# Optimization experiments

Measured on AMD Instinct MI355X. Metric: run time of the kernel, lower is better.

The kernel has to match this reference:

```python
import jax, jax.numpy as jnp
import numpy as np

B, N, E, H = 8, 2000, 20, 128


def setup_inputs() -> dict:
    key = jax.random.key(0)
    ks = jax.random.split(key, 9)
    s = 1.0 / np.sqrt(H)
    return {
        "x": jax.random.normal(ks[0], (B, N, H), dtype=jnp.float32),
        "e": jax.random.normal(ks[1], (B, N * E, H), dtype=jnp.float32),
        "Wu": jax.random.uniform(ks[2], (H, H), jnp.float32, -s, s),
        "bu": jax.random.uniform(ks[3], (H,), jnp.float32, -s, s),
        "Wv": jax.random.uniform(ks[4], (H, H), jnp.float32, -s, s),
        "bv": jax.random.uniform(ks[5], (H,), jnp.float32, -s, s),
        "We": jax.random.uniform(ks[6], (H, H), jnp.float32, -s, s),
        "be": jax.random.uniform(ks[7], (H,), jnp.float32, -s, s),
        "edge_index": jax.random.randint(ks[8], (B, N * E), 0, N, dtype=jnp.int32),
        "n_edges": E,
    }


def reference(x, e, Wu, bu, Wv, bv, We, be, edge_index, n_edges):
    b, n, h = x.shape
    Ux = x @ Wu + bu                      # [B, N, H] node self-embedding
    Vx = x @ Wv + bv                      # [B, N, H] neighbor embedding
    Ve = e @ We + be                      # [B, N*E, H] edge embedding
    # softmax over the n_edges axis per (node, channel)
    Ve = jax.nn.softmax(Ve.reshape(b, n, n_edges, h), axis=2)
    # gather neighbor features along node axis via edge_index
    Vx_g = jnp.take_along_axis(Vx, edge_index[..., None], axis=1)  # [B, N*E, H]
    to = (Ve * Vx_g.reshape(b, n, n_edges, h)).sum(axis=2)          # [B, N, H]
    return Ux + to
```

## Files before the change

kernel.cpp:

```cpp
#include <hip/hip_runtime.h>

#define B_   8
#define NN   2000
#define EE   20
#define HH   128
#define BN   (B_*NN)
#define NE   (NN*EE)

typedef unsigned short ushort_t;
typedef __bf16 bf16x8 __attribute__((ext_vector_type(8)));
typedef float  f32x4  __attribute__((ext_vector_type(4)));
typedef float  f4     __attribute__((ext_vector_type(4)));
typedef unsigned short us8 __attribute__((ext_vector_type(8)));
typedef unsigned short us4 __attribute__((ext_vector_type(4)));

union FragU { us8 u; bf16x8 b; };

__device__ __forceinline__ float b2f(ushort_t v) {
    union { unsigned int i; float f; } c; c.i = ((unsigned int)v) << 16; return c.f;
}
__device__ __forceinline__ ushort_t f2b(float f) {
    union { float f; unsigned int i; } c; c.f = f;
    unsigned int r = (c.i + 0x7FFFu + ((c.i >> 16) & 1u)) >> 16;
    return (ushort_t)r;
}

__global__ __launch_bounds__(256, 2) void k1_embed(
    const float* __restrict__ x,
    const float* __restrict__ Wu, const float* __restrict__ bu,
    const float* __restrict__ Wv, const float* __restrict__ bv,
    ushort_t* __restrict__ Uxb, ushort_t* __restrict__ Vxb)
{
    __shared__ __align__(16) ushort_t As[128 * 136];

    const int tid  = threadIdx.x;
    const int lane = tid & 63;
    const int wave = tid >> 6;
    const int wm = wave >> 1, wn = wave & 1;
    const int q  = lane >> 4, ln = lane & 15;
    const int m0 = blockIdx.x * 128;
    const int sel = blockIdx.y;
    const float* W    = sel ? Wv : Wu;
    const float* bias = sel ? bv : bu;
    ushort_t* dst = sel ? Vxb : Uxb;

    for (int c = tid; c < 128 * 32; c += 256) {
        int row = c >> 5, col = (c & 31) * 4;
        f4 v = *(const f4*)(x + (size_t)(m0 + row) * HH + col);
        us4 pk;
#pragma unroll
        for (int r = 0; r < 4; ++r) pk[r] = f2b(v[r]);
        *(us4*)(&As[row * 136 + col]) = pk;
    }

    FragU bf[4][4];
#pragma unroll
    for (int ki = 0; ki < 4; ++ki)
#pragma unroll
        for (int tn = 0; tn < 4; ++tn) {
            int n = wn * 64 + tn * 16 + ln;
            us8 tmp;
#pragma unroll
            for (int i = 0; i < 8; ++i) tmp[i] = f2b(W[(ki * 32 + q * 8 + i) * HH + n]);
            bf[ki][tn].u = tmp;
        }

    f32x4 acc[4][4];
#pragma unroll
    for (int tm = 0; tm < 4; ++tm)
#pragma unroll
        for (int tn = 0; tn < 4; ++tn) acc[tm][tn] = (f32x4){0.f, 0.f, 0.f, 0.f};

    __syncthreads();

#pragma unroll
    for (int ki = 0; ki < 4; ++ki) {
        FragU af[4];
#pragma unroll
        for (int tm = 0; tm < 4; ++tm) {
            int row = wm * 64 + tm * 16 + ln;
            af[tm].u = *(const us8*)(&As[row * 136 + ki * 32 + q * 8]);
        }
#pragma unroll
        for (int tm = 0; tm < 4; ++tm)
#pragma unroll
            for (int tn = 0; tn < 4; ++tn)
                acc[tm][tn] = __builtin_amdgcn_mfma_f32_16x16x32_bf16(
                    af[tm].b, bf[ki][tn].b, acc[tm][tn], 0, 0, 0);
    }

#pragma unroll
    for (int tn = 0; tn < 4; ++tn) {
        int col = wn * 64 + tn * 16 + ln;
        float bb = bias[col];
#pragma unroll
        for (int tm = 0; tm < 4; ++tm) {
            int rowb = m0 + wm * 64 + tm * 16 + q * 4;
#pragma unroll
            for (int r = 0; r < 4; ++r) {
                float v = acc[tm][tn][r] + bb;
                dst[(size_t)(rowb + r) * HH + col] = f2b(v);
            }
        }
    }
}

__global__ __launch_bounds__(256, 2) void k2_fused(
    const float* __restrict__ e, const float* __restrict__ We,
    const int* __restrict__ eidx,
    const ushort_t* __restrict__ Uxb, const ushort_t* __restrict__ Vxb,
    float* __restrict__ out)
{
    __shared__ __align__(16) ushort_t smem[160 * 136];
    __shared__ int sidx[160];

    const int tid  = threadIdx.x;
    const int lane = tid & 63;
    const int wave = tid >> 6;
    const int wm = wave >> 1, wn = wave & 1;
    const int q  = lane >> 4, ln = lane & 15;

    const int node0 = blockIdx.x * 8;
    const int b   = node0 / NN;
    const int nl0 = node0 - b * NN;
    const size_t erow0 = (size_t)b * NE + (size_t)nl0 * EE;

    for (int c = tid; c < 160 * 32; c += 256) {
        int row = c >> 5, col = (c & 31) * 4;
        f4 v = *(const f4*)(e + (erow0 + row) * HH + col);
        us4 pk;
#pragma unroll
        for (int r = 0; r < 4; ++r) pk[r] = f2b(v[r]);
        *(us4*)(&smem[row * 136 + col]) = pk;
    }
    if (tid < 160) sidx[tid] = eidx[erow0 + tid];

    FragU bf[4][4];
#pragma unroll
    for (int ki = 0; ki < 4; ++ki)
#pragma unroll
        for (int tn = 0; tn < 4; ++tn) {
            int n = wn * 64 + tn * 16 + ln;
            us8 tmp;
#pragma unroll
            for (int i = 0; i < 8; ++i) tmp[i] = f2b(We[(ki * 32 + q * 8 + i) * HH + n]);
            bf[ki][tn].u = tmp;
        }

    f32x4 acc[5][4];
#pragma unroll
    for (int tm = 0; tm < 5; ++tm)
#pragma unroll
        for (int tn = 0; tn < 4; ++tn) acc[tm][tn] = (f32x4){0.f, 0.f, 0.f, 0.f};

    __syncthreads();

#pragma unroll
    for (int ki = 0; ki < 4; ++ki) {
        FragU af[5];
#pragma unroll
        for (int tm = 0; tm < 5; ++tm) {
            int row = wm * 80 + tm * 16 + ln;
            af[tm].u = *(const us8*)(&smem[row * 136 + ki * 32 + q * 8]);
        }
#pragma unroll
        for (int tm = 0; tm < 5; ++tm)
#pragma unroll
            for (int tn = 0; tn < 4; ++tn)
                acc[tm][tn] = __builtin_amdgcn_mfma_f32_16x16x32_bf16(
                    af[tm].b, bf[ki][tn].b, acc[tm][tn], 0, 0, 0);
    }

    __syncthreads();

#pragma unroll
    for (int tm = 0; tm < 5; ++tm)
#pragma unroll
        for (int tn = 0; tn < 4; ++tn) {
            int col  = wn * 64 + tn * 16 + ln;
            int rowb = wm * 80 + tm * 16 + q * 4;
            us4 pk;
#pragma unroll
            for (int r = 0; r < 4; ++r) pk[r] = f2b(acc[tm][tn][r]);
            *(us4*)(&smem[col * 168 + rowb]) = pk;
        }

    __syncthreads();

    const int h  = tid & 127;
    const int gp = tid >> 7;
#pragma unroll 1
    for (int j = 0; j < 4; ++j) {
        int g = gp + 2 * j;
        const ushort_t* ctp = &smem[h * 168 + g * 20];
        float lv[20];
#pragma unroll
        for (int i = 0; i < 5; ++i) {
            us4 v = *(const us4*)(ctp + i * 4);
#pragma unroll
            for (int r = 0; r < 4; ++r) lv[i * 4 + r] = b2f(v[r]);
        }
        float mx = lv[0];
#pragma unroll
        for (int k = 1; k < EE; ++k) mx = fmaxf(mx, lv[k]);

        ushort_t gv[20];
        const int ib = g * 20;
#pragma unroll
        for (int k = 0; k < EE; ++k)
            gv[k] = Vxb[(size_t)(b * NN + sidx[ib + k]) * HH + h];

        float s = 0.f, a = 0.f;
#pragma unroll
        for (int k = 0; k < EE; ++k) {
            float p = __expf(lv[k] - mx);
            s += p;
            a = fmaf(p, b2f(gv[k]), a);
        }
        size_t orow = (size_t)(node0 + g) * HH + h;
        out[orow] = b2f(Uxb[orow]) + a / s;
    }
}

extern "C" void kernel_launch(void* const* d_in, const int* in_sizes, int n_in,
                              void* d_out, int out_size, void* d_ws, size_t ws_size,
                              hipStream_t stream) {
    const float* x  = (const float*)d_in[0];
    const float* e  = (const float*)d_in[1];
    const float* Wu = (const float*)d_in[2];
    const float* bu = (const float*)d_in[3];
    const float* Wv = (const float*)d_in[4];
    const float* bv = (const float*)d_in[5];
    const float* We = (const float*)d_in[6];
    const int*   eidx = (const int*)d_in[8];

    ushort_t* Uxb = (ushort_t*)d_ws;
    ushort_t* Vxb = (ushort_t*)((char*)d_ws + (size_t)BN * HH * 2);
    float*    o   = (float*)d_out;

    k1_embed<<<dim3(125, 2), 256, 0, stream>>>(x, Wu, bu, Wv, bv, Uxb, Vxb);
    k2_fused<<<dim3(2000), 256, 0, stream>>>(e, We, eidx, Uxb, Vxb, o);
}
```

Baseline: 300.0 us.

## Halve tile sizes, load k1 A-fragments directly, raise k2 occupancy

k1 now processes 64 rows per block and loads the x fragments straight from global memory into registers, dropping the LDS staging and the barrier. k2 handles 4 nodes (80 edges) per block on a 2D grid, with each wave covering 32 output columns, a smaller LDS footprint and a transposed-stride change, and its launch bound is raised to 4 blocks per CU. The aim is more resident blocks and more parallelism to hide the latency of the memory-bound e stream and the gather. The cost is that each block now loads its weight fragments for half as much work, so the We/W loading and bf16 conversion overhead doubles in relative terms.

```diff
diff --git a/kernel.cpp b/kernel.cpp
--- a/kernel.cpp
+++ b/kernel.cpp
@@ -25,33 +25,36 @@
     return (ushort_t)r;
 }
 
-__global__ __launch_bounds__(256, 2) void k1_embed(
+__global__ __launch_bounds__(256) void k1_embed(
     const float* __restrict__ x,
     const float* __restrict__ Wu, const float* __restrict__ bu,
     const float* __restrict__ Wv, const float* __restrict__ bv,
     ushort_t* __restrict__ Uxb, ushort_t* __restrict__ Vxb)
 {
-    __shared__ __align__(16) ushort_t As[128 * 136];
-
     const int tid  = threadIdx.x;
     const int lane = tid & 63;
     const int wave = tid >> 6;
     const int wm = wave >> 1, wn = wave & 1;
     const int q  = lane >> 4, ln = lane & 15;
-    const int m0 = blockIdx.x * 128;
+    const int m0 = blockIdx.x * 64;
     const int sel = blockIdx.y;
     const float* W    = sel ? Wv : Wu;
     const float* bias = sel ? bv : bu;
     ushort_t* dst = sel ? Vxb : Uxb;
 
-    for (int c = tid; c < 128 * 32; c += 256) {
-        int row = c >> 5, col = (c & 31) * 4;
-        f4 v = *(const f4*)(x + (size_t)(m0 + row) * HH + col);
-        us4 pk;
-#pragma unroll
-        for (int r = 0; r < 4; ++r) pk[r] = f2b(v[r]);
-        *(us4*)(&As[row * 136 + col]) = pk;
-    }
+    FragU af[2][4];
+#pragma unroll
+    for (int tm = 0; tm < 2; ++tm)
+#pragma unroll
+        for (int ki = 0; ki < 4; ++ki) {
+            const float* p = x + (size_t)(m0 + wm * 32 + tm * 16 + ln) * HH + ki * 32 + q * 8;
+            f4 lo = *(const f4*)(p);
+            f4 hi = *(const f4*)(p + 4);
+            us8 t;
+#pragma unroll
+            for (int r = 0; r < 4; ++r) { t[r] = f2b(lo[r]); t[r + 4] = f2b(hi[r]); }
+            af[tm][ki].u = t;
+        }
 
     FragU bf[4][4];
 #pragma unroll
@@ -59,99 +62,89 @@
 #pragma unroll
         for (int tn = 0; tn < 4; ++tn) {
             int n = wn * 64 + tn * 16 + ln;
-            us8 tmp;
-#pragma unroll
-            for (int i = 0; i < 8; ++i) tmp[i] = f2b(W[(ki * 32 + q * 8 + i) * HH + n]);
-            bf[ki][tn].u = tmp;
-        }
-
-    f32x4 acc[4][4];
-#pragma unroll
-    for (int tm = 0; tm < 4; ++tm)
+            us8 t;
+#pragma unroll
+            for (int i = 0; i < 8; ++i) t[i] = f2b(W[(ki * 32 + q * 8 + i) * HH + n]);
+            bf[ki][tn].u = t;
+        }
+
+    f32x4 acc[2][4];
+#pragma unroll
+    for (int tm = 0; tm < 2; ++tm)
 #pragma unroll
         for (int tn = 0; tn < 4; ++tn) acc[tm][tn] = (f32x4){0.f, 0.f, 0.f, 0.f};
 
-    __syncthreads();
-
-#pragma unroll
-    for (int ki = 0; ki < 4; ++ki) {
-        FragU af[4];
-#pragma unroll
-        for (int tm = 0; tm < 4; ++tm) {
-            int row = wm * 64 + tm * 16 + ln;
-            af[tm].u = *(const us8*)(&As[row * 136 + ki * 32 + q * 8]);
-        }
-#pragma unroll
-        for (int tm = 0; tm < 4; ++tm)
+#pragma unroll
+    for (int ki = 0; ki < 4; ++ki)
+#pragma unroll
+        for (int tm = 0; tm < 2; ++tm)
 #pragma unroll
             for (int tn = 0; tn < 4; ++tn)
                 acc[tm][tn] = __builtin_amdgcn_mfma_f32_16x16x32_bf16(
-                    af[tm].b, bf[ki][tn].b, acc[tm][tn], 0, 0, 0);
-    }
+                    af[tm][ki].b, bf[ki][tn].b, acc[tm][tn], 0, 0, 0);
 
 #pragma unroll
     for (int tn = 0; tn < 4; ++tn) {
         int col = wn * 64 + tn * 16 + ln;
         float bb = bias[col];
 #pragma unroll
-        for (int tm = 0; tm < 4; ++tm) {
-            int rowb = m0 + wm * 64 + tm * 16 + q * 4;
-#pragma unroll
-            for (int r = 0; r < 4; ++r) {
-                float v = acc[tm][tn][r] + bb;
-                dst[(size_t)(rowb + r) * HH + col] = f2b(v);
-            }
-        }
-    }
-}
-
-__global__ __launch_bounds__(256, 2) void k2_fused(
+        for (int tm = 0; tm < 2; ++tm) {
+            int rowb = m0 + wm * 32 + tm * 16 + q * 4;
+#pragma unroll
+            for (int r = 0; r < 4; ++r)
+                dst[(size_t)(rowb + r) * HH + col] = f2b(acc[tm][tn][r] + bb);
+        }
+    }
+}
+
+#define ASTR 136
+#define CSTR 84
+
+__global__ __launch_bounds__(256, 4) void k2_fused(
     const float* __restrict__ e, const float* __restrict__ We,
     const int* __restrict__ eidx,
     const ushort_t* __restrict__ Uxb, const ushort_t* __restrict__ Vxb,
     float* __restrict__ out)
 {
-    __shared__ __align__(16) ushort_t smem[160 * 136];
-    __shared__ int sidx[160];
+    __shared__ __align__(16) ushort_t smem[11008];
+    __shared__ int sidx[80];
 
     const int tid  = threadIdx.x;
     const int lane = tid & 63;
     const int wave = tid >> 6;
-    const int wm = wave >> 1, wn = wave & 1;
     const int q  = lane >> 4, ln = lane & 15;
 
-    const int node0 = blockIdx.x * 8;
-    const int b   = node0 / NN;
-    const int nl0 = node0 - b * NN;
+    const int b   = blockIdx.y;
+    const int nl0 = blockIdx.x * 4;
     const size_t erow0 = (size_t)b * NE + (size_t)nl0 * EE;
 
-    for (int c = tid; c < 160 * 32; c += 256) {
+    for (int c = tid; c < 80 * 32; c += 256) {
         int row = c >> 5, col = (c & 31) * 4;
         f4 v = *(const f4*)(e + (erow0 + row) * HH + col);
         us4 pk;
 #pragma unroll
         for (int r = 0; r < 4; ++r) pk[r] = f2b(v[r]);
-        *(us4*)(&smem[row * 136 + col]) = pk;
-    }
-    if (tid < 160) sidx[tid] = eidx[erow0 + tid];
-
-    FragU bf[4][4];
+        *(us4*)(&smem[row * ASTR + col]) = pk;
+    }
+    if (tid < 80) sidx[tid] = eidx[erow0 + tid];
+
+    FragU bf[4][2];
 #pragma unroll
     for (int ki = 0; ki < 4; ++ki)
 #pragma unroll
-        for (int tn = 0; tn < 4; ++tn) {
-            int n = wn * 64 + tn * 16 + ln;
-            us8 tmp;
-#pragma unroll
-            for (int i = 0; i < 8; ++i) tmp[i] = f2b(We[(ki * 32 + q * 8 + i) * HH + n]);
-            bf[ki][tn].u = tmp;
-        }
-
-    f32x4 acc[5][4];
+        for (int tn = 0; tn < 2; ++tn) {
+            int n = wave * 32 + tn * 16 + ln;
+            us8 t;
+#pragma unroll
+            for (int i = 0; i < 8; ++i) t[i] = f2b(We[(ki * 32 + q * 8 + i) * HH + n]);
+            bf[ki][tn].u = t;
+        }
+
+    f32x4 acc[5][2];
 #pragma unroll
     for (int tm = 0; tm < 5; ++tm)
 #pragma unroll
-        for (int tn = 0; tn < 4; ++tn) acc[tm][tn] = (f32x4){0.f, 0.f, 0.f, 0.f};
+        for (int tn = 0; tn < 2; ++tn) acc[tm][tn] = (f32x4){0.f, 0.f, 0.f, 0.f};
 
     __syncthreads();
 
@@ -159,14 +152,12 @@
     for (int ki = 0; ki < 4; ++ki) {
         FragU af[5];
 #pragma unroll
-        for (int tm = 0; tm < 5; ++tm) {
-            int row = wm * 80 + tm * 16 + ln;
-            af[tm].u = *(const us8*)(&smem[row * 136 + ki * 32 + q * 8]);
-        }
-#pragma unroll
         for (int tm = 0; tm < 5; ++tm)
-#pragma unroll
-            for (int tn = 0; tn < 4; ++tn)
+            af[tm].u = *(const us8*)(&smem[(tm * 16 + ln) * ASTR + ki * 32 + q * 8]);
+#pragma unroll
+        for (int tm = 0; tm < 5; ++tm)
+#pragma unroll
+            for (int tn = 0; tn < 2; ++tn)
                 acc[tm][tn] = __builtin_amdgcn_mfma_f32_16x16x32_bf16(
                     af[tm].b, bf[ki][tn].b, acc[tm][tn], 0, 0, 0);
     }
@@ -176,13 +167,13 @@
 #pragma unroll
     for (int tm = 0; tm < 5; ++tm)
 #pragma unroll
-        for (int tn = 0; tn < 4; ++tn) {
-            int col  = wn * 64 + tn * 16 + ln;
-            int rowb = wm * 80 + tm * 16 + q * 4;
+        for (int tn = 0; tn < 2; ++tn) {
+            int col  = wave * 32 + tn * 16 + ln;
+            int rowb = tm * 16 + q * 4;
             us4 pk;
 #pragma unroll
             for (int r = 0; r < 4; ++r) pk[r] = f2b(acc[tm][tn][r]);
-            *(us4*)(&smem[col * 168 + rowb]) = pk;
+            *(us4*)(&smem[col * CSTR + rowb]) = pk;
         }
 
     __syncthreads();
@@ -190,9 +181,9 @@
     const int h  = tid & 127;
     const int gp = tid >> 7;
 #pragma unroll 1
-    for (int j = 0; j < 4; ++j) {
+    for (int j = 0; j < 2; ++j) {
         int g = gp + 2 * j;
-        const ushort_t* ctp = &smem[h * 168 + g * 20];
+        const ushort_t* ctp = &smem[h * CSTR + g * 20];
         float lv[20];
 #pragma unroll
         for (int i = 0; i < 5; ++i) {
@@ -217,7 +208,7 @@
             s += p;
             a = fmaf(p, b2f(gv[k]), a);
         }
-        size_t orow = (size_t)(node0 + g) * HH + h;
+        size_t orow = (size_t)(b * NN + nl0 + g) * HH + h;
         out[orow] = b2f(Uxb[orow]) + a / s;
     }
 }
@@ -238,6 +229,6 @@
     ushort_t* Vxb = (ushort_t*)((char*)d_ws + (size_t)BN * HH * 2);
     float*    o   = (float*)d_out;
 
-    k1_embed<<<dim3(125, 2), 256, 0, stream>>>(x, Wu, bu, Wv, bv, Uxb, Vxb);
-    k2_fused<<<dim3(2000), 256, 0, stream>>>(e, We, eidx, Uxb, Vxb, o);
-}
+    k1_embed<<<dim3(250, 2), 256, 0, stream>>>(x, Wu, bu, Wv, bv, Uxb, Vxb);
+    k2_fused<<<dim3(500, 8), 256, 0, stream>>>(e, We, eidx, Uxb, Vxb, o);
+}
```

Measured after the change: 275.7 us. -8.1%, faster.
